# Performance work log

Measured on AMD Instinct MI355X. Metric: run time of the kernel, lower is better.

Reference implementation:

```python
import math
import jax, jax.numpy as jnp
import numpy as np

NUM_BUCKETS = 32
MAX_DISTANCE = 128
N_HEADS = 16
D_KV = 64


def _relative_position_bucket(rel_pos, num_buckets=NUM_BUCKETS, max_distance=MAX_DISTANCE):
    # bidirectional=True branch of T5's bucketing
    num_buckets = num_buckets // 2
    rel_buckets = (rel_pos > 0).astype(jnp.int32) * num_buckets
    rel_pos = jnp.abs(rel_pos)
    max_exact = num_buckets // 2
    is_small = rel_pos < max_exact
    # safe log (values < max_exact are masked out by is_small)
    rp_f = jnp.maximum(rel_pos, 1).astype(jnp.float32)
    rel_if_large = max_exact + (
        jnp.log(rp_f / max_exact) / math.log(max_distance / max_exact) * (num_buckets - max_exact)
    ).astype(jnp.int32)
    rel_if_large = jnp.minimum(rel_if_large, num_buckets - 1)
    return rel_buckets + jnp.where(is_small, rel_pos, rel_if_large)


def compute_bias(rel_bias_table, q_len, k_len):
    ctx = jnp.arange(q_len)[:, None]
    mem = jnp.arange(k_len)[None, :]
    buckets = _relative_position_bucket(mem - ctx)  # [q, k]
    values = rel_bias_table[buckets]                # [q, k, h]
    return jnp.transpose(values, (2, 0, 1))[None]   # [1, h, q, k]


def setup_inputs() -> dict:
    key = jax.random.key(0)
    k1, k2, k3, k4 = jax.random.split(key, 4)
    d_model = 1024
    return {
        "hidden_states": jax.random.normal(k1, (2, 2048, d_model), jnp.float32),
        "w_qkv": jax.random.normal(k2, (d_model, 3 * N_HEADS * D_KV), jnp.float32) * (d_model ** -0.5),
        "w_o": jax.random.normal(k3, (N_HEADS * D_KV, d_model), jnp.float32) * ((N_HEADS * D_KV) ** -0.5),
        "rel_bias_table": jax.random.normal(k4, (NUM_BUCKETS, N_HEADS), jnp.float32),
    }


def reference(hidden_states, w_qkv, w_o, rel_bias_table):
    b, s, _ = hidden_states.shape
    inner = N_HEADS * D_KV
    qkv = hidden_states @ w_qkv                         # [b, s, 3*inner]
    q, k, v = jnp.split(qkv, [inner, 2 * inner], axis=-1)
    def to_bhsd(x):
        return jnp.transpose(x.reshape(b, s, N_HEADS, D_KV), (0, 2, 1, 3))
    q, k, v = to_bhsd(q), to_bhsd(k), to_bhsd(v)
    scores = jnp.einsum("bhqd,bhkd->bhqk", q, k)        # no 1/sqrt(d) scaling in T5
    position_bias = compute_bias(rel_bias_table, s, s)  # [1, h, q, k]
    scores = scores + position_bias
    attn = jax.nn.softmax(scores.astype(jnp.float32), axis=-1).astype(scores.dtype)
    out = jnp.einsum("bhqk,bhkd->bhqd", attn, v)
    out = jnp.transpose(out, (0, 2, 1, 3)).reshape(b, s, inner)
    attn_output = out @ w_o
    return attn_output, position_bias
```

## Files before the change

### kernel.cpp

```cpp
#include <hip/hip_runtime.h>
#include <hip/hip_bf16.h>
#include <cstdint>
#include <cstddef>

#define S_LEN 2048
#define NH 16
#define DKV 64
#define BATCH 2
#define DMODEL 1024

typedef _Float16 half_t;
typedef __attribute__((ext_vector_type(4))) _Float16 halfx4;
typedef __attribute__((ext_vector_type(8))) _Float16 half8;
typedef __attribute__((ext_vector_type(4))) float floatx4;

__device__ __forceinline__ void load_lds16(const half_t* g, half_t* l) {
  __builtin_amdgcn_global_load_lds((const __attribute__((address_space(1))) void*)g,
                                   (__attribute__((address_space(3))) void*)l, 16, 0, 0);
}

__device__ __forceinline__ float qmax16(float v) {
  int i;
  i = __builtin_amdgcn_ds_swizzle(__float_as_int(v), 0x041F); v = fmaxf(v, __int_as_float(i));
  i = __builtin_amdgcn_ds_swizzle(__float_as_int(v), 0x081F); v = fmaxf(v, __int_as_float(i));
  i = __builtin_amdgcn_ds_swizzle(__float_as_int(v), 0x101F); v = fmaxf(v, __int_as_float(i));
  i = __builtin_amdgcn_ds_swizzle(__float_as_int(v), 0x201F); v = fmaxf(v, __int_as_float(i));
  return v;
}

__device__ __forceinline__ int t5_bucket(int delta) {
  int base = (delta > 0) ? 16 : 0;
  int a = delta < 0 ? -delta : delta;
  int n;
  if (a < 8)       n = a;
  else if (a < 12) n = 8;
  else if (a < 16) n = 9;
  else if (a < 23) n = 10;
  else if (a < 32) n = 11;
  else if (a < 46) n = 12;
  else if (a < 64) n = 13;
  else if (a < 91) n = 14;
  else             n = 15;
  return base + n;
}

__global__ __launch_bounds__(256) void bias_kernel(const float* __restrict__ table,
                                                   float* __restrict__ out) {
  int h = blockIdx.x >> 11;
  int q = blockIdx.x & (S_LEN - 1);
  __shared__ float tb[32];
  if (threadIdx.x < 32) tb[threadIdx.x] = table[threadIdx.x * NH + h];
  __syncthreads();
  float* dst = out + (size_t)blockIdx.x * S_LEN;
  int k0 = threadIdx.x * 4;
#pragma unroll
  for (int half = 0; half < 2; half++) {
    int k = k0 + half * 1024;
    float4 v;
    v.x = tb[t5_bucket((k + 0) - q)];
    v.y = tb[t5_bucket((k + 1) - q)];
    v.z = tb[t5_bucket((k + 2) - q)];
    v.w = tb[t5_bucket((k + 3) - q)];
    *(float4*)(dst + k) = v;
  }
}

__global__ __launch_bounds__(256) void cast_f2h(const float* __restrict__ in,
                                                half_t* __restrict__ out) {
  int i = blockIdx.x * 256 + threadIdx.x;
  float4 v = ((const float4*)in)[i];
  halfx4 h;
  h[0] = (half_t)v.x; h[1] = (half_t)v.y; h[2] = (half_t)v.z; h[3] = (half_t)v.w;
  ((halfx4*)out)[i] = h;
}

__global__ __launch_bounds__(256) void transpose_cast(const float* __restrict__ in,
                                                      half_t* __restrict__ out,
                                                      int R, int C) {
  __shared__ float t[32][33];
  int lr = threadIdx.x >> 3;
  int lc = (threadIdx.x & 7) * 4;
  int r0 = blockIdx.y * 32, c0 = blockIdx.x * 32;
  float4 v = *(const float4*)(in + (size_t)(r0 + lr) * C + c0 + lc);
  t[lr][lc + 0] = v.x; t[lr][lc + 1] = v.y; t[lr][lc + 2] = v.z; t[lr][lc + 3] = v.w;
  __syncthreads();
  halfx4 hv;
#pragma unroll
  for (int u = 0; u < 4; u++) hv[u] = (half_t)t[lc + u][lr];
  *(halfx4*)(out + (size_t)(c0 + lr) * R + r0 + lc) = hv;
}

__global__ __launch_bounds__(256) void vtrans(const half_t* __restrict__ V,
                                              half_t* __restrict__ Vt) {
  __shared__ half_t T[64 * 72];
  const int bh = blockIdx.y;
  const int s0 = blockIdx.x * 64;
  const half_t* src = V + ((size_t)bh * S_LEN + s0) * DKV;
  half_t* dst = Vt + (size_t)bh * DKV * S_LEN + s0;
  const int sr = threadIdx.x >> 3;
  const int dc = (threadIdx.x & 7) * 8;
#pragma unroll
  for (int p = 0; p < 2; p++) {
    int s = sr + p * 32;
    half8 v = *(const half8*)(src + (size_t)s * DKV + dc);
#pragma unroll
    for (int u = 0; u < 8; u++) T[(dc + u) * 72 + s] = v[u];
  }
  __syncthreads();
#pragma unroll
  for (int p = 0; p < 2; p++) {
    int d = sr + p * 32;
    half8 v = *(half8*)&T[d * 72 + dc];
    *(half8*)(dst + (size_t)d * S_LEN + dc) = v;
  }
}

template <int MODE>
__global__ __launch_bounds__(256) void hgemm128(const half_t* __restrict__ A,
                                                const half_t* __restrict__ Bt,
                                                float* __restrict__ C,
                                                half_t* __restrict__ Qo,
                                                half_t* __restrict__ Ko,
                                                half_t* __restrict__ Vo,
                                                int M, int N, int K) {
  __shared__ half_t Asl[8 * 512];
  __shared__ half_t Bsl[8 * 512];

  const int tid = threadIdx.x;
  const int w = tid >> 6;
  const int lane = tid & 63;
  const int l15 = lane & 15;
  const int quad = lane >> 4;
  const int wm = w >> 1, wn = w & 1;
  const int m0 = blockIdx.y * 128;
  const int n0 = blockIdx.x * 128;

  floatx4 acc[4][4];
#pragma unroll
  for (int i = 0; i < 4; i++)
#pragma unroll
    for (int j = 0; j < 4; j++) acc[i][j] = (floatx4){0.f, 0.f, 0.f, 0.f};

  const half_t* ga0 = A + (size_t)(m0 + (2 * w + 0) * 16 + l15) * K + quad * 8;
  const half_t* ga1 = A + (size_t)(m0 + (2 * w + 1) * 16 + l15) * K + quad * 8;
  const half_t* gb0 = Bt + (size_t)(n0 + (2 * w + 0) * 16 + l15) * K + quad * 8;
  const half_t* gb1 = Bt + (size_t)(n0 + (2 * w + 1) * 16 + l15) * K + quad * 8;
  half_t* la0 = &Asl[(2 * w + 0) * 512];
  half_t* la1 = &Asl[(2 * w + 1) * 512];
  half_t* lb0 = &Bsl[(2 * w + 0) * 512];
  half_t* lb1 = &Bsl[(2 * w + 1) * 512];

  for (int k0 = 0; k0 < K; k0 += 32) {
    __syncthreads();
    load_lds16(ga0 + k0, la0);
    load_lds16(ga1 + k0, la1);
    load_lds16(gb0 + k0, lb0);
    load_lds16(gb1 + k0, lb1);
    __syncthreads();

    half8 af[4], bf[4];
#pragma unroll
    for (int i = 0; i < 4; i++) af[i] = *(half8*)&Asl[(wm * 4 + i) * 512 + lane * 8];
#pragma unroll
    for (int j = 0; j < 4; j++) bf[j] = *(half8*)&Bsl[(wn * 4 + j) * 512 + lane * 8];
#pragma unroll
    for (int i = 0; i < 4; i++)
#pragma unroll
      for (int j = 0; j < 4; j++)
        acc[i][j] = __builtin_amdgcn_mfma_f32_16x16x32_f16(af[i], bf[j], acc[i][j], 0, 0, 0);
  }

  const int rowbase = m0 + wm * 64;
  const int colbase = n0 + wn * 64;
  if (MODE == 0) {
#pragma unroll
    for (int i = 0; i < 4; i++)
#pragma unroll
      for (int j = 0; j < 4; j++)
#pragma unroll
        for (int r = 0; r < 4; r++)
          C[(size_t)(rowbase + i * 16 + quad * 4 + r) * N + colbase + j * 16 + l15] =
              acc[i][j][r];
  } else {
    const int which = colbase >> 10;
    const int h = (colbase & 1023) >> 6;
    const int b = rowbase >> 11;
    const int s0 = rowbase & (S_LEN - 1);
    half_t* base = ((which == 0) ? Qo : (which == 1) ? Ko : Vo) +
                   (size_t)(b * NH + h) * S_LEN * DKV;
#pragma unroll
    for (int i = 0; i < 4; i++)
#pragma unroll
      for (int j = 0; j < 4; j++)
#pragma unroll
        for (int r = 0; r < 4; r++)
          base[(size_t)(s0 + i * 16 + quad * 4 + r) * DKV + j * 16 + l15] =
              (half_t)acc[i][j][r];
  }
}

__global__ __launch_bounds__(256) void attn_split(const half_t* __restrict__ Q,
                                                  const half_t* __restrict__ K,
                                                  const half_t* __restrict__ Vt,
                                                  const float* __restrict__ table,
                                                  float* __restrict__ Opart,
                                                  float* __restrict__ Mp,
                                                  float* __restrict__ Lp) {
  __shared__ half_t Ks[64 * 64];
  __shared__ half_t Vts[64 * 64];
  __shared__ half_t Ps[64 * 68];
  __shared__ float tb[32];
  __shared__ float badd[184];

  const int tid = threadIdx.x;
  const int w = tid >> 6;
  const int lane = tid & 63;
  const int l15 = lane & 15;
  const int quad = lane >> 4;
  const int bh = blockIdx.y;
  const int h = bh & (NH - 1);
  const int part = blockIdx.x & 1;
  const int q0w = (blockIdx.x >> 1) * 64 + w * 16;

  if (tid < 32) tb[tid] = table[tid * NH + h];
  __syncthreads();
  if (tid < 183) badd[tid] = tb[t5_bucket(tid - 91)];
  const float tb_neg = tb[15], tb_pos = tb[31];

  half8 qf[2];
#pragma unroll
  for (int ks = 0; ks < 2; ks++)
    qf[ks] = *(const half8*)(Q + ((size_t)bh * S_LEN + q0w + l15) * DKV +
                             ks * 32 + quad * 8);

  half8 bones;
#pragma unroll
  for (int j = 0; j < 8; j++) bones[j] = (l15 == 0) ? (half_t)1.0f : (half_t)0.0f;

  floatx4 o[4], oL;
  float m[4];
#pragma unroll
  for (int r = 0; r < 4; r++) m[r] = -1e30f;
#pragma unroll
  for (int nb = 0; nb < 4; nb++) o[nb] = (floatx4){0.f, 0.f, 0.f, 0.f};
  oL = (floatx4){0.f, 0.f, 0.f, 0.f};

  const int jr = tid >> 2;
  const int ub = (tid & 3) * 2;
  const int sw = jr & 7;
  const int kv_rd0 = l15 * 64 + ((0 * 4 + quad) ^ (l15 & 7)) * 8;
  const int kv_rd1 = l15 * 64 + ((1 * 4 + quad) ^ (l15 & 7)) * 8;
  const int ps_wr = (w * 16 + quad * 4) * 68 + l15;
  const int ps_rd = (w * 16 + l15) * 68 + quad * 8;

  const half_t* Kg = K + ((size_t)bh * S_LEN + part * 1024 + jr) * DKV + ub * 8;
  const half_t* Vg = Vt + ((size_t)bh * DKV + jr) * S_LEN + part * 1024 + ub * 8;
  int rel = part * 1024 - q0w;

  for (int it = 0; it < 16; it++, rel += 64, Kg += 64 * DKV, Vg += 64) {
    __syncthreads();
    {
      half8 k0v = *(const half8*)(Kg);
      half8 k1v = *(const half8*)(Kg + 8);
      half8 v0v = *(const half8*)(Vg);
      half8 v1v = *(const half8*)(Vg + 8);
      *(half8*)&Ks[jr * 64 + ((ub + 0) ^ sw) * 8] = k0v;
      *(half8*)&Ks[jr * 64 + ((ub + 1) ^ sw) * 8] = k1v;
      *(half8*)&Vts[jr * 64 + ((ub + 0) ^ sw) * 8] = v0v;
      *(half8*)&Vts[jr * 64 + ((ub + 1) ^ sw) * 8] = v1v;
    }
    __syncthreads();

    floatx4 s[4];
#pragma unroll
    for (int nb = 0; nb < 4; nb++) {
      s[nb] = (floatx4){0.f, 0.f, 0.f, 0.f};
      s[nb] = __builtin_amdgcn_mfma_f32_16x16x32_f16(
          qf[0], *(half8*)&Ks[nb * 1024 + kv_rd0], s[nb], 0, 0, 0);
      s[nb] = __builtin_amdgcn_mfma_f32_16x16x32_f16(
          qf[1], *(half8*)&Ks[nb * 1024 + kv_rd1], s[nb], 0, 0, 0);
    }

    float al[4];
    if (rel >= 106 || rel <= -154) {
      const float lb = (rel >= 106) ? tb_pos : tb_neg;
#pragma unroll
      for (int r = 0; r < 4; r++) {
        float cm = qmax16(fmaxf(fmaxf(s[0][r], s[1][r]), fmaxf(s[2][r], s[3][r])));
        float mn = fmaxf(m[r], cm);
        al[r] = __expf(m[r] - mn);
        m[r] = mn;
        float sh = lb - mn;
#pragma unroll
        for (int nb = 0; nb < 4; nb++)
          Ps[ps_wr + r * 68 + nb * 16] = (half_t)__expf(s[nb][r] + sh);
#pragma unroll
        for (int nb = 0; nb < 4; nb++) o[nb][r] *= al[r];
        oL[r] *= al[r];
      }
    } else {
#pragma unroll
      for (int r = 0; r < 4; r++) {
        int db = rel + l15 - (quad * 4 + r) + 91;
        float bv[4];
#pragma unroll
        for (int nb = 0; nb < 4; nb++) {
          int idx = db + nb * 16;
          idx = idx < 0 ? 0 : (idx > 182 ? 182 : idx);
          bv[nb] = badd[idx];
        }
        float cm = qmax16(fmaxf(fmaxf(s[0][r], s[1][r]), fmaxf(s[2][r], s[3][r])));
        float mn = fmaxf(m[r], cm);
        al[r] = __expf(m[r] - mn);
        m[r] = mn;
#pragma unroll
        for (int nb = 0; nb < 4; nb++)
          Ps[ps_wr + r * 68 + nb * 16] = (half_t)__expf(s[nb][r] - mn + bv[nb]);
#pragma unroll
        for (int nb = 0; nb < 4; nb++) o[nb][r] *= al[r];
        oL[r] *= al[r];
      }
    }

    half8 af0 = *(half8*)&Ps[ps_rd];
    half8 af1 = *(half8*)&Ps[ps_rd + 32];
#pragma unroll
    for (int nb = 0; nb < 4; nb++) {
      o[nb] = __builtin_amdgcn_mfma_f32_16x16x32_f16(
          af0, *(half8*)&Vts[nb * 1024 + kv_rd0], o[nb], 0, 0, 0);
      o[nb] = __builtin_amdgcn_mfma_f32_16x16x32_f16(
          af1, *(half8*)&Vts[nb * 1024 + kv_rd1], o[nb], 0, 0, 0);
    }
    oL = __builtin_amdgcn_mfma_f32_16x16x32_f16(af0, bones, oL, 0, 0, 0);
    oL = __builtin_amdgcn_mfma_f32_16x16x32_f16(af1, bones, oL, 0, 0, 0);
  }

#pragma unroll
  for (int r = 0; r < 4; r++) {
    int row = bh * S_LEN + q0w + quad * 4 + r;
    float* op = Opart + (size_t)part * 4194304 + (size_t)row * 64;
#pragma unroll
    for (int nb = 0; nb < 4; nb++) op[nb * 16 + l15] = o[nb][r];
    if (l15 == 0) {
      Mp[part * 65536 + row] = m[r];
      Lp[part * 65536 + row] = oL[r];
    }
  }
}

__global__ __launch_bounds__(256) void attn_combine(const float* __restrict__ Opart,
                                                    const float* __restrict__ Mp,
                                                    const float* __restrict__ Lp,
                                                    half_t* __restrict__ X) {
  int idx = blockIdx.x * 256 + threadIdx.x;
  int row = idx >> 6;
  int d = idx & 63;
  float m0 = Mp[row], m1 = Mp[65536 + row];
  float l0 = Lp[row], l1 = Lp[65536 + row];
  float M = fmaxf(m0, m1);
  float a0 = __expf(m0 - M), a1 = __expf(m1 - M);
  float L = l0 * a0 + l1 * a1;
  float o = (Opart[(size_t)row * 64 + d] * a0 +
             Opart[4194304 + (size_t)row * 64 + d] * a1) / L;
  int bh = row >> 11, q = row & (S_LEN - 1);
  int b = bh >> 4, h = bh & (NH - 1);
  X[(size_t)(b * S_LEN + q) * DMODEL + h * DKV + d] = (half_t)o;
}

extern "C" void kernel_launch(void* const* d_in, const int* in_sizes, int n_in,
                              void* d_out, int out_size, void* d_ws, size_t ws_size,
                              hipStream_t stream) {
  const float* hidden = (const float*)d_in[0];
  const float* w_qkv = (const float*)d_in[1];
  const float* w_o = (const float*)d_in[2];
  const float* table = (const float*)d_in[3];

  float* attn_out = (float*)d_out;
  float* bias_out = (float*)d_out + 4194304;

  half_t* Ah  = (half_t*)d_ws;
  half_t* Wqt = Ah + 4194304;
  half_t* Wot = Wqt + 3145728;
  half_t* Qh  = Wot + 1048576;
  half_t* Kh  = Qh + 4194304;
  half_t* Vh  = Kh + 4194304;
  half_t* Xh  = Vh + 4194304;
  half_t* Vth = Ah;
  float* Opart = (float*)(Xh + 4194304);
  float* Mpp   = Opart + 8388608;
  float* Lpp   = Mpp + 131072;

  cast_f2h<<<4096, 256, 0, stream>>>(hidden, Ah);
  transpose_cast<<<dim3(3072 / 32, 1024 / 32), 256, 0, stream>>>(w_qkv, Wqt, 1024, 3072);
  transpose_cast<<<dim3(1024 / 32, 1024 / 32), 256, 0, stream>>>(w_o, Wot, 1024, 1024);
  bias_kernel<<<NH * S_LEN, 256, 0, stream>>>(table, bias_out);

  hgemm128<1><<<dim3(3072 / 128, 4096 / 128), 256, 0, stream>>>(
      Ah, Wqt, nullptr, Qh, Kh, Vh, 4096, 3072, 1024);

  vtrans<<<dim3(S_LEN / 64, BATCH * NH), 256, 0, stream>>>(Vh, Vth);

  attn_split<<<dim3((S_LEN / 64) * 2, BATCH * NH), 256, 0, stream>>>(
      Qh, Kh, Vth, table, Opart, Mpp, Lpp);
  attn_combine<<<4194304 / 256, 256, 0, stream>>>(Opart, Mpp, Lpp, Xh);

  hgemm128<0><<<dim3(1024 / 128, 4096 / 128), 256, 0, stream>>>(
      Xh, Wot, attn_out, nullptr, nullptr, nullptr, 4096, 1024, 1024);
}
```

Before: 502.9 us.

## Compute transposed scores to keep P in registers and use exp2 softmax

The attention kernel swaps the MFMA operands so each lane holds one query row's scores. That lets the P matrix feed the PV MFMA straight from registers (16x16x16), removing the Ps shared-memory round trip and the extra ones-vector MFMA for the row sum. The row max and sum now use one swizzle plus one shuffle instead of per-row 16-lane reductions. Q and the bias table are pre-scaled by log2(e) so exp2 can replace exp, with slight fp16 rounding differences in Q.

```diff
diff --git a/kernel.cpp b/kernel.cpp
--- a/kernel.cpp
+++ b/kernel.cpp
@@ -8,6 +8,7 @@
 #define DKV 64
 #define BATCH 2
 #define DMODEL 1024
+#define LOG2E 1.4426950408889634f
 
 typedef _Float16 half_t;
 typedef __attribute__((ext_vector_type(4))) _Float16 halfx4;
@@ -17,15 +18,6 @@
 __device__ __forceinline__ void load_lds16(const half_t* g, half_t* l) {
   __builtin_amdgcn_global_load_lds((const __attribute__((address_space(1))) void*)g,
                                    (__attribute__((address_space(3))) void*)l, 16, 0, 0);
-}
-
-__device__ __forceinline__ float qmax16(float v) {
-  int i;
-  i = __builtin_amdgcn_ds_swizzle(__float_as_int(v), 0x041F); v = fmaxf(v, __int_as_float(i));
-  i = __builtin_amdgcn_ds_swizzle(__float_as_int(v), 0x081F); v = fmaxf(v, __int_as_float(i));
-  i = __builtin_amdgcn_ds_swizzle(__float_as_int(v), 0x101F); v = fmaxf(v, __int_as_float(i));
-  i = __builtin_amdgcn_ds_swizzle(__float_as_int(v), 0x201F); v = fmaxf(v, __int_as_float(i));
-  return v;
 }
 
 __device__ __forceinline__ int t5_bucket(int delta) {
@@ -186,6 +178,7 @@
     const int h = (colbase & 1023) >> 6;
     const int b = rowbase >> 11;
     const int s0 = rowbase & (S_LEN - 1);
+    const float scale = (which == 0) ? LOG2E : 1.0f;
     half_t* base = ((which == 0) ? Qo : (which == 1) ? Ko : Vo) +
                    (size_t)(b * NH + h) * S_LEN * DKV;
 #pragma unroll
@@ -195,7 +188,7 @@
 #pragma unroll
         for (int r = 0; r < 4; r++)
           base[(size_t)(s0 + i * 16 + quad * 4 + r) * DKV + j * 16 + l15] =
-              (half_t)acc[i][j][r];
+              (half_t)(acc[i][j][r] * scale);
   }
 }
 
@@ -208,7 +201,6 @@
                                                   float* __restrict__ Lp) {
   __shared__ half_t Ks[64 * 64];
   __shared__ half_t Vts[64 * 64];
-  __shared__ half_t Ps[64 * 68];
   __shared__ float tb[32];
   __shared__ float badd[184];
 
@@ -222,7 +214,7 @@
   const int part = blockIdx.x & 1;
   const int q0w = (blockIdx.x >> 1) * 64 + w * 16;
 
-  if (tid < 32) tb[tid] = table[tid * NH + h];
+  if (tid < 32) tb[tid] = table[tid * NH + h] * LOG2E;
   __syncthreads();
   if (tid < 183) badd[tid] = tb[t5_bucket(tid - 91)];
   const float tb_neg = tb[15], tb_pos = tb[31];
@@ -233,25 +225,17 @@
     qf[ks] = *(const half8*)(Q + ((size_t)bh * S_LEN + q0w + l15) * DKV +
                              ks * 32 + quad * 8);
 
-  half8 bones;
-#pragma unroll
-  for (int j = 0; j < 8; j++) bones[j] = (l15 == 0) ? (half_t)1.0f : (half_t)0.0f;
-
-  floatx4 o[4], oL;
-  float m[4];
-#pragma unroll
-  for (int r = 0; r < 4; r++) m[r] = -1e30f;
+  floatx4 o[4];
 #pragma unroll
   for (int nb = 0; nb < 4; nb++) o[nb] = (floatx4){0.f, 0.f, 0.f, 0.f};
-  oL = (floatx4){0.f, 0.f, 0.f, 0.f};
+  float m = -1e30f, l = 0.0f;
 
   const int jr = tid >> 2;
   const int ub = (tid & 3) * 2;
   const int sw = jr & 7;
   const int kv_rd0 = l15 * 64 + ((0 * 4 + quad) ^ (l15 & 7)) * 8;
   const int kv_rd1 = l15 * 64 + ((1 * 4 + quad) ^ (l15 & 7)) * 8;
-  const int ps_wr = (w * 16 + quad * 4) * 68 + l15;
-  const int ps_rd = (w * 16 + l15) * 68 + quad * 8;
+  const int q2h = quad >> 1, q2l = (quad & 1) * 4;
 
   const half_t* Kg = K + ((size_t)bh * S_LEN + part * 1024 + jr) * DKV + ub * 8;
   const half_t* Vg = Vt + ((size_t)bh * DKV + jr) * S_LEN + part * 1024 + ub * 8;
@@ -276,74 +260,82 @@
     for (int nb = 0; nb < 4; nb++) {
       s[nb] = (floatx4){0.f, 0.f, 0.f, 0.f};
       s[nb] = __builtin_amdgcn_mfma_f32_16x16x32_f16(
-          qf[0], *(half8*)&Ks[nb * 1024 + kv_rd0], s[nb], 0, 0, 0);
+          *(half8*)&Ks[nb * 1024 + kv_rd0], qf[0], s[nb], 0, 0, 0);
       s[nb] = __builtin_amdgcn_mfma_f32_16x16x32_f16(
-          qf[1], *(half8*)&Ks[nb * 1024 + kv_rd1], s[nb], 0, 0, 0);
-    }
-
-    float al[4];
+          *(half8*)&Ks[nb * 1024 + kv_rd1], qf[1], s[nb], 0, 0, 0);
+    }
+
+    float cm = fmaxf(fmaxf(fmaxf(s[0][0], s[0][1]), fmaxf(s[0][2], s[0][3])),
+                     fmaxf(fmaxf(s[1][0], s[1][1]), fmaxf(s[1][2], s[1][3])));
+    cm = fmaxf(cm, fmaxf(fmaxf(fmaxf(s[2][0], s[2][1]), fmaxf(s[2][2], s[2][3])),
+                         fmaxf(fmaxf(s[3][0], s[3][1]), fmaxf(s[3][2], s[3][3]))));
+    {
+      int i = __builtin_amdgcn_ds_swizzle(__float_as_int(cm), 0x401F);
+      cm = fmaxf(cm, __int_as_float(i));
+      cm = fmaxf(cm, __shfl_xor(cm, 32));
+    }
+    float mn = fmaxf(m, cm);
+    float al = exp2f(m - mn);
+    m = mn;
+
+    float lsum = 0.0f;
+    halfx4 pvb[4];
     if (rel >= 106 || rel <= -154) {
-      const float lb = (rel >= 106) ? tb_pos : tb_neg;
-#pragma unroll
-      for (int r = 0; r < 4; r++) {
-        float cm = qmax16(fmaxf(fmaxf(s[0][r], s[1][r]), fmaxf(s[2][r], s[3][r])));
-        float mn = fmaxf(m[r], cm);
-        al[r] = __expf(m[r] - mn);
-        m[r] = mn;
-        float sh = lb - mn;
-#pragma unroll
-        for (int nb = 0; nb < 4; nb++)
-          Ps[ps_wr + r * 68 + nb * 16] = (half_t)__expf(s[nb][r] + sh);
-#pragma unroll
-        for (int nb = 0; nb < 4; nb++) o[nb][r] *= al[r];
-        oL[r] *= al[r];
+      const float sh = ((rel >= 106) ? tb_pos : tb_neg) - mn;
+#pragma unroll
+      for (int nb = 0; nb < 4; nb++)
+#pragma unroll
+        for (int r = 0; r < 4; r++) {
+          float p = exp2f(s[nb][r] + sh);
+          lsum += p;
+          pvb[nb][r] = (half_t)p;
+        }
+    } else {
+      const int db = rel + quad * 4 - l15 + 91;
+#pragma unroll
+      for (int nb = 0; nb < 4; nb++)
+#pragma unroll
+        for (int r = 0; r < 4; r++) {
+          int idx = db + nb * 16 + r;
+          idx = idx < 0 ? 0 : (idx > 182 ? 182 : idx);
+          float p = exp2f(s[nb][r] - mn + badd[idx]);
+          lsum += p;
+          pvb[nb][r] = (half_t)p;
+        }
+    }
+    {
+      int i = __builtin_amdgcn_ds_swizzle(__float_as_int(lsum), 0x401F);
+      lsum += __int_as_float(i);
+      lsum += __shfl_xor(lsum, 32);
+    }
+    l = l * al + lsum;
+#pragma unroll
+    for (int nb = 0; nb < 4; nb++)
+#pragma unroll
+      for (int r = 0; r < 4; r++) o[nb][r] *= al;
+
+#pragma unroll
+    for (int nb = 0; nb < 4; nb++) {
+      const int vrow = (nb * 16 + l15);
+      const int vsw = vrow & 7;
+#pragma unroll
+      for (int kt = 0; kt < 4; kt++) {
+        halfx4 vf = *(halfx4*)&Vts[vrow * 64 + ((kt * 2 + q2h) ^ vsw) * 8 + q2l];
+        o[nb] = __builtin_amdgcn_mfma_f32_16x16x16f16(vf, pvb[kt], o[nb], 0, 0, 0);
       }
-    } else {
-#pragma unroll
-      for (int r = 0; r < 4; r++) {
-        int db = rel + l15 - (quad * 4 + r) + 91;
-        float bv[4];
-#pragma unroll
-        for (int nb = 0; nb < 4; nb++) {
-          int idx = db + nb * 16;
-          idx = idx < 0 ? 0 : (idx > 182 ? 182 : idx);
-          bv[nb] = badd[idx];
-        }
-        float cm = qmax16(fmaxf(fmaxf(s[0][r], s[1][r]), fmaxf(s[2][r], s[3][r])));
-        float mn = fmaxf(m[r], cm);
-        al[r] = __expf(m[r] - mn);
-        m[r] = mn;
-#pragma unroll
-        for (int nb = 0; nb < 4; nb++)
-          Ps[ps_wr + r * 68 + nb * 16] = (half_t)__expf(s[nb][r] - mn + bv[nb]);
-#pragma unroll
-        for (int nb = 0; nb < 4; nb++) o[nb][r] *= al[r];
-        oL[r] *= al[r];
-      }
-    }
-
-    half8 af0 = *(half8*)&Ps[ps_rd];
-    half8 af1 = *(half8*)&Ps[ps_rd + 32];
-#pragma unroll
-    for (int nb = 0; nb < 4; nb++) {
-      o[nb] = __builtin_amdgcn_mfma_f32_16x16x32_f16(
-          af0, *(half8*)&Vts[nb * 1024 + kv_rd0], o[nb], 0, 0, 0);
-      o[nb] = __builtin_amdgcn_mfma_f32_16x16x32_f16(
-          af1, *(half8*)&Vts[nb * 1024 + kv_rd1], o[nb], 0, 0, 0);
-    }
-    oL = __builtin_amdgcn_mfma_f32_16x16x32_f16(af0, bones, oL, 0, 0, 0);
-    oL = __builtin_amdgcn_mfma_f32_16x16x32_f16(af1, bones, oL, 0, 0, 0);
-  }
-
-#pragma unroll
-  for (int r = 0; r < 4; r++) {
-    int row = bh * S_LEN + q0w + quad * 4 + r;
+    }
+  }
+
+  {
+    int row = bh * S_LEN + q0w + l15;
     float* op = Opart + (size_t)part * 4194304 + (size_t)row * 64;
 #pragma unroll
-    for (int nb = 0; nb < 4; nb++) op[nb * 16 + l15] = o[nb][r];
-    if (l15 == 0) {
-      Mp[part * 65536 + row] = m[r];
-      Lp[part * 65536 + row] = oL[r];
+    for (int nb = 0; nb < 4; nb++)
+      *(float4*)(op + nb * 16 + quad * 4) =
+          make_float4(o[nb][0], o[nb][1], o[nb][2], o[nb][3]);
+    if (quad == 0) {
+      Mp[part * 65536 + row] = m;
+      Lp[part * 65536 + row] = l;
     }
   }
 }
@@ -358,7 +350,7 @@
   float m0 = Mp[row], m1 = Mp[65536 + row];
   float l0 = Lp[row], l1 = Lp[65536 + row];
   float M = fmaxf(m0, m1);
-  float a0 = __expf(m0 - M), a1 = __expf(m1 - M);
+  float a0 = exp2f(m0 - M), a1 = exp2f(m1 - M);
   float L = l0 * a0 + l1 * a1;
   float o = (Opart[(size_t)row * 64 + d] * a0 +
              Opart[4194304 + (size_t)row * 64 + d] * a1) / L;
```

Measured after the change: 497.5 us. No clear change (-1.1%).
